# Performance work log

Measured on AMD Instinct MI355X. Metric: run time of the kernel, lower is better.

## Reference

```python
import jax, jax.numpy as jnp
import numpy as np

N_NODES = 100000
N_EDGES = 1600000
D_IN = 64
D_HID = 64


def setup_inputs() -> dict:
    key = jax.random.key(0)
    ks = jax.random.split(key, 9)
    feat = jax.random.uniform(ks[0], (N_NODES, D_IN), dtype=jnp.float32) + 1e-3
    edge_index = jax.random.randint(ks[1], (2, N_EDGES), 0, N_NODES, dtype=jnp.int64)
    edge_vals = jax.random.uniform(ks[2], (N_EDGES,), dtype=jnp.float32) + 1e-3
    W1 = jax.random.normal(ks[3], (D_IN, D_HID), dtype=jnp.float32) * 0.1
    b1 = jax.random.normal(ks[4], (D_HID,), dtype=jnp.float32) * 0.1
    W2 = jax.random.normal(ks[5], (D_HID, D_HID), dtype=jnp.float32) * 0.1
    b2 = jax.random.normal(ks[6], (D_HID,), dtype=jnp.float32) * 0.1
    W3 = jax.random.normal(ks[7], (D_HID, 1), dtype=jnp.float32) * 0.1
    b3 = jax.random.normal(ks[8], (1,), dtype=jnp.float32) * 0.1
    return {"feat": feat, "edge_index": edge_index, "edge_vals": edge_vals,
            "W1": W1, "b1": b1, "W2": W2, "b2": b2, "W3": W3, "b3": b3}


def reference(feat, edge_index, edge_vals, W1, b1, W2, b2, W3, b3):
    N = feat.shape[0]
    src = edge_index[0]
    dst = edge_index[1]
    # --- __init__: A_hat = D^{-1} A D^{-1}, D = diag(row sums of A) ---
    deg_row = jax.ops.segment_sum(edge_vals, src, num_segments=N)
    deg_row = jnp.where(deg_row > 0, deg_row, 1.0)  # guard isolated nodes
    w_hat = edge_vals / (deg_row[src] * deg_row[dst])  # A_hat edge weights
    # --- GCNConv gcn_norm: add self loops (weight 1), symmetric D^{-1/2} norm ---
    loops = jnp.arange(N, dtype=src.dtype)
    row = jnp.concatenate([src, loops])   # message sources
    col = jnp.concatenate([dst, loops])   # message targets (aggregation index)
    w = jnp.concatenate([w_hat, jnp.ones((N,), dtype=feat.dtype)])
    deg = jax.ops.segment_sum(w, col, num_segments=N)
    dinv = jnp.where(deg > 0, jax.lax.rsqrt(deg), 0.0)
    norm = dinv[row] * w * dinv[col]      # [E+N]

    def gcn_conv(x, W, b):
        h = x @ W                          # [N, d_out]
        msg = norm[:, None] * h[row]       # gather + scale, [E+N, d_out]
        return jax.ops.segment_sum(msg, col, num_segments=N) + b

    # --- forward ---
    x = feat / jnp.sum(feat, axis=1, keepdims=True)
    x = jax.nn.relu(gcn_conv(x, W1, b1))
    x = jax.nn.relu(gcn_conv(x, W2, b2))
    x = gcn_conv(x, W3, b3)               # final layer, no activation
    return x
```

## Files before the change

### kernel.cpp

```cpp
#include <hip/hip_runtime.h>
#include <hip/hip_fp16.h>


#define CAP    48
#define NRL    256
#define NBMX   512
#define P0E    2048

#define PG     2048

__device__ __forceinline__ float dec_ev(unsigned pk) {
    return __half2float(__ushort_as_half((unsigned short)(pk >> 17)));
}
__device__ __forceinline__ float dec_ev15(unsigned pk) {
    return __half2float(__ushort_as_half((unsigned short)(pk & 0x7FFF)));
}

__global__ __launch_bounds__(256) void k_scatter(
        const int* __restrict__ src, const int* __restrict__ dst,
        const float* __restrict__ ev,
        int* __restrict__ meta_d, int2* __restrict__ part_blk,
        int* __restrict__ meta_s, int* __restrict__ parts_src,
        int E, int NB) {
    __shared__ int2 srt[P0E];
    __shared__ int  srs[P0E];
    __shared__ int hd[NBMX], cbd[NBMX], lod[NBMX];
    __shared__ int hs[NBMX], cbs[NBMX], los[NBMX];
    int bx = (int)blockIdx.x, tid = (int)threadIdx.x;
    int e0 = bx * P0E;
    int ne = E - e0; if (ne > P0E) ne = P0E; if (ne < 0) ne = 0;
    for (int i = tid; i < NB; i += 256) { hd[i] = 0; hs[i] = 0; }
    __syncthreads();
    for (int i = tid; i < ne; i += 256) {
        atomicAdd(&hd[dst[e0 + i] >> 8], 1);
        atomicAdd(&hs[src[e0 + i] >> 8], 1);
    }
    __syncthreads();
    int wv = tid >> 6, ln = tid & 63;
    if (wv < 2) {
        int* h  = wv ? hs  : hd;
        int* cb = wv ? cbs : cbd;
        int run = 0;
        #pragma unroll
        for (int k = 0; k < NBMX / 64; k++) {
            int idx = k * 64 + ln;
            int v = (idx < NB) ? h[idx] : 0;
            int sc = v;
            #pragma unroll
            for (int o = 1; o < 64; o <<= 1) {
                int u = __shfl_up(sc, o, 64);
                if (ln >= o) sc += u;
            }
            if (idx < NB) cb[idx] = run + sc - v;
            run += __shfl(sc, 63, 64);
        }
    }
    __syncthreads();
    for (int c = tid; c < NB; c += 256) {
        lod[c] = cbd[c];
        los[c] = cbs[c];
        meta_d[(size_t)bx * NB + c] = (cbd[c] << 16) | hd[c];
        meta_s[(size_t)bx * NB + c] = (cbs[c] << 16) | hs[c];
    }
    __syncthreads();
    for (int i = tid; i < ne; i += 256) {
        int e = e0 + i;
        int s = src[e], d = dst[e];
        float v = ev[e];
        unsigned evh = (unsigned)__half_as_ushort(__float2half_rn(v)) & 0x7FFF;
        int p = atomicAdd(&lod[d >> 8], 1);
        int2 r;
        r.x = ((d & (NRL - 1)) << 17) | s;
        r.y = __float_as_int(v);
        srt[p] = r;
        int q = atomicAdd(&los[s >> 8], 1);
        srs[q] = (int)(((unsigned)(s & (NRL - 1)) << 15) | evh);
    }
    __syncthreads();
    for (int i = tid; i < ne; i += 256) {
        part_blk[(size_t)bx * P0E + i]  = srt[i];
        parts_src[(size_t)bx * P0E + i] = srs[i];
    }
}

__global__ __launch_bounds__(256) void k_degacc(
        const int* __restrict__ parts_src, const int* __restrict__ meta_s,
        float* __restrict__ deg_row, int N, int NB, int nsb) {
    __shared__ float dl[NRL];
    int b = (int)blockIdx.x, tid = (int)threadIdx.x;
    if (tid < NRL) dl[tid] = 0.f;
    __syncthreads();
    for (int bx = tid; bx < nsb; bx += 256) {
        int m = meta_s[(size_t)bx * NB + b];
        int base = m >> 16, len = m & 0xFFFF;
        const int* seg = parts_src + (size_t)bx * P0E + base;
        for (int j = 0; j < len; j++) {
            unsigned pk = (unsigned)seg[j];
            atomicAdd(&dl[pk >> 15], dec_ev15(pk));
        }
    }
    __syncthreads();
    int node = (b << 8) + tid;
    if (tid < NRL && node < N) deg_row[node] = dl[tid];
}

__global__ __launch_bounds__(256) void k_gemm1(
        const float* __restrict__ feat, const float* __restrict__ W1,
        __half* __restrict__ B, int N) {
    int lane = threadIdx.x & 63;
    float w[64];
    #pragma unroll
    for (int k = 0; k < 64; k++) w[k] = W1[k * 64 + lane];
    int wid = (int)blockIdx.x * 4 + (threadIdx.x >> 6);
    const int nw = PG * 4;
    for (int node = wid; node < N; node += nw) {
        float v = feat[(size_t)node * 64 + lane];
        float s = v;
        #pragma unroll
        for (int o = 1; o < 64; o <<= 1) s += __shfl_xor(s, o, 64);
        int myb = __float_as_int(v / s);
        float a0 = 0.f, a1 = 0.f, a2 = 0.f, a3 = 0.f;
        #pragma unroll
        for (int k = 0; k < 64; k += 4) {
            a0 = fmaf(__int_as_float(__builtin_amdgcn_readlane(myb, k + 0)), w[k + 0], a0);
            a1 = fmaf(__int_as_float(__builtin_amdgcn_readlane(myb, k + 1)), w[k + 1], a1);
            a2 = fmaf(__int_as_float(__builtin_amdgcn_readlane(myb, k + 2)), w[k + 2], a2);
            a3 = fmaf(__int_as_float(__builtin_amdgcn_readlane(myb, k + 3)), w[k + 3], a3);
        }
        B[(size_t)node * 64 + lane] = __float2half((a0 + a1) + (a2 + a3));
    }
}

__global__ __launch_bounds__(256) void k_bucket(
        const int2* __restrict__ part_blk, const int* __restrict__ meta_d,
        const float* __restrict__ deg_row,
        int* __restrict__ cnt, int* __restrict__ epair,
        float* __restrict__ di_t, float* __restrict__ r_t,
        int N, int NB, int nsb) {
    __shared__ int   lbuck[NRL * CAP];
    __shared__ int   lcnt[NRL];
    __shared__ float lt[NRL];
    int b = (int)blockIdx.x, tid = (int)threadIdx.x;
    if (tid < NRL) { lcnt[tid] = 0; lt[tid] = 0.f; }
    __syncthreads();
    for (int bx = tid; bx < nsb; bx += 256) {
        int m = meta_d[(size_t)bx * NB + b];
        int base = m >> 16, len = m & 0xFFFF;
        const int2* seg = part_blk + (size_t)bx * P0E + base;
        for (int j = 0; j < len; j++) {
            int2 r = seg[j];
            int dl = (r.x >> 17) & (NRL - 1);
            int s  = r.x & 0x1FFFF;
            float v = __int_as_float(r.y);
            atomicAdd(&lt[dl], v / deg_row[s]);
            unsigned evh = (unsigned)__half_as_ushort(__float2half_rn(v)) & 0x7FFF;
            int p = atomicAdd(&lcnt[dl], 1);
            if (p < CAP) lbuck[dl * CAP + p] = (int)((evh << 17) | (unsigned)s);
        }
    }
    __syncthreads();
    int node0 = b << 8;
    if (tid < NRL) {
        int node = node0 + tid;
        if (node < N) {
            int c = lcnt[tid]; if (c > CAP) c = CAP;
            cnt[node] = c;
            float drd = deg_row[node];
            drd = drd > 0.f ? drd : 1.f;
            float qd = 1.0f / drd;
            float di = rsqrtf(1.0f + qd * lt[tid]);
            di_t[node] = di;
            r_t[node]  = qd * di;
        }
    }
    __syncthreads();
    size_t base = (size_t)node0 * CAP;
    for (int i = tid; i < NRL * CAP; i += 256) epair[base + i] = lbuck[i];
}

__global__ __launch_bounds__(256) void k_p3(const int* __restrict__ cnt,
                                            int* __restrict__ epair,
                                            const float* __restrict__ r_t, int N) {
    int lane = threadIdx.x & 63;
    int node = blockIdx.x * 4 + (threadIdx.x >> 6);
    if (node >= N) return;
    int c = cnt[node]; if (c > CAP) c = CAP;
    if (lane < c) {
        size_t o = (size_t)node * CAP + lane;
        unsigned e = (unsigned)epair[o];
        int s = (int)(e & 0x1FFFF);
        float w = dec_ev(e) * r_t[s];
        unsigned wh = (unsigned)__half_as_ushort(__float2half_rn(w)) & 0x7FFF;
        epair[o] = (int)((wh << 17) | (unsigned)s);
    }
}

__device__ __forceinline__ void gather8(int c, int rec,
        const __half* __restrict__ h, int grp, int sub, float acc[8]) {
    #pragma unroll
    for (int q = 0; q < 8; q++) acc[q] = 0.f;
    int nb = (c + 7) >> 3;
    for (int t = 0; t < nb; t += 2) {
        int r0 = __shfl(rec, (t << 3) + grp, 64);
        int s0 = r0 & 0x1FFFF;
        float w0 = dec_ev((unsigned)r0);
        uint4 d0 = *reinterpret_cast<const uint4*>(h + ((size_t)s0 << 6) + (sub << 3));
        bool have1 = (t + 1 < nb);
        uint4 d1; float w1 = 0.f;
        if (have1) {
            int r1 = __shfl(rec, (t << 3) + 8 + grp, 64);
            int s1 = r1 & 0x1FFFF;
            w1 = dec_ev((unsigned)r1);
            d1 = *reinterpret_cast<const uint4*>(h + ((size_t)s1 << 6) + (sub << 3));
        }
        {
            const __half2* p0 = reinterpret_cast<const __half2*>(&d0);
            #pragma unroll
            for (int q = 0; q < 4; q++) {
                float2 f = __half22float2(p0[q]);
                acc[2 * q]     = fmaf(w0, f.x, acc[2 * q]);
                acc[2 * q + 1] = fmaf(w0, f.y, acc[2 * q + 1]);
            }
        }
        if (have1) {
            const __half2* p1 = reinterpret_cast<const __half2*>(&d1);
            #pragma unroll
            for (int q = 0; q < 4; q++) {
                float2 f = __half22float2(p1[q]);
                acc[2 * q]     = fmaf(w1, f.x, acc[2 * q]);
                acc[2 * q + 1] = fmaf(w1, f.y, acc[2 * q + 1]);
            }
        }
    }
    #pragma unroll
    for (int o = 8; o < 64; o <<= 1) {
        #pragma unroll
        for (int q = 0; q < 8; q++)
            acc[q] += __shfl_xor(acc[q], o, 64);
    }
}

__global__ __launch_bounds__(256) void k_gath1(
        const int* __restrict__ cnt, const int* __restrict__ epair,
        const __half* __restrict__ B,
        const float* __restrict__ di_t, const float* __restrict__ r_t,
        const float* __restrict__ b1, __half* __restrict__ X2, int N) {
    int lane = threadIdx.x & 63;
    int grp = lane >> 3, sub = lane & 7;
    int node = (int)blockIdx.x * 4 + (threadIdx.x >> 6);
    if (node >= N) return;
    int un = __builtin_amdgcn_readfirstlane(node);
    int c  = __builtin_amdgcn_readfirstlane(cnt[un]);
    if (c > CAP) c = CAP;
    int rec = 0;
    if (lane < c) rec = epair[(size_t)un * CAP + lane];
    uint4 dow = *reinterpret_cast<const uint4*>(B + ((size_t)un << 6) + (sub << 3));
    float g[8];
    gather8(c, rec, B, grp, sub, g);
    float di = di_t[un], rd = r_t[un];
    float dd = di * di;
    const float4* b4 = reinterpret_cast<const float4*>(b1);
    float4 bA = b4[sub * 2], bB = b4[sub * 2 + 1];
    const __half2* po = reinterpret_cast<const __half2*>(&dow);
    float2 o0 = __half22float2(po[0]), o1 = __half22float2(po[1]);
    float2 o2 = __half22float2(po[2]), o3 = __half22float2(po[3]);
    float x0 = fmaxf(bA.x + dd * o0.x + rd * g[0], 0.f);
    float x1 = fmaxf(bA.y + dd * o0.y + rd * g[1], 0.f);
    float x2 = fmaxf(bA.z + dd * o1.x + rd * g[2], 0.f);
    float x3 = fmaxf(bA.w + dd * o1.y + rd * g[3], 0.f);
    float x4 = fmaxf(bB.x + dd * o2.x + rd * g[4], 0.f);
    float x5 = fmaxf(bB.y + dd * o2.y + rd * g[5], 0.f);
    float x6 = fmaxf(bB.z + dd * o3.x + rd * g[6], 0.f);
    float x7 = fmaxf(bB.w + dd * o3.y + rd * g[7], 0.f);
    if (grp == 0) {
        __half2 h0 = __floats2half2_rn(x0, x1);
        __half2 h1 = __floats2half2_rn(x2, x3);
        __half2 h2 = __floats2half2_rn(x4, x5);
        __half2 h3 = __floats2half2_rn(x6, x7);
        uint4 ov;
        ov.x = *reinterpret_cast<unsigned*>(&h0);
        ov.y = *reinterpret_cast<unsigned*>(&h1);
        ov.z = *reinterpret_cast<unsigned*>(&h2);
        ov.w = *reinterpret_cast<unsigned*>(&h3);
        *reinterpret_cast<uint4*>(X2 + ((size_t)un << 6) + (sub << 3)) = ov;
    }
}

__global__ __launch_bounds__(256) void k_gemm2(
        const __half* __restrict__ X2, const float* __restrict__ W2,
        __half* __restrict__ C, int N) {
    int lane = threadIdx.x & 63;
    float w[64];
    #pragma unroll
    for (int k = 0; k < 64; k++) w[k] = W2[k * 64 + lane];
    int wid = (int)blockIdx.x * 4 + (threadIdx.x >> 6);
    const int nw = PG * 4;
    for (int node = wid; node < N; node += nw) {
        int myb = __float_as_int(__half2float(X2[(size_t)node * 64 + lane]));
        float a0 = 0.f, a1 = 0.f, a2 = 0.f, a3 = 0.f;
        #pragma unroll
        for (int k = 0; k < 64; k += 4) {
            a0 = fmaf(__int_as_float(__builtin_amdgcn_readlane(myb, k + 0)), w[k + 0], a0);
            a1 = fmaf(__int_as_float(__builtin_amdgcn_readlane(myb, k + 1)), w[k + 1], a1);
            a2 = fmaf(__int_as_float(__builtin_amdgcn_readlane(myb, k + 2)), w[k + 2], a2);
            a3 = fmaf(__int_as_float(__builtin_amdgcn_readlane(myb, k + 3)), w[k + 3], a3);
        }
        C[(size_t)node * 64 + lane] = __float2half((a0 + a1) + (a2 + a3));
    }
}

__global__ __launch_bounds__(256) void k_gather_dot(
        const int* __restrict__ cnt, const int* __restrict__ epair,
        const __half* __restrict__ C,
        const float* __restrict__ di_t, const float* __restrict__ r_t,
        const float* __restrict__ b2, const float* __restrict__ W3,
        float* __restrict__ h3, int N) {
    int lane = threadIdx.x & 63;
    int grp = lane >> 3, sub = lane & 7;
    int node = (int)blockIdx.x * 4 + (threadIdx.x >> 6);
    if (node >= N) return;
    int un = __builtin_amdgcn_readfirstlane(node);
    int c  = __builtin_amdgcn_readfirstlane(cnt[un]);
    if (c > CAP) c = CAP;
    int rec = 0;
    if (lane < c) rec = epair[(size_t)un * CAP + lane];
    uint4 dow = *reinterpret_cast<const uint4*>(C + ((size_t)un << 6) + (sub << 3));
    float g[8];
    gather8(c, rec, C, grp, sub, g);
    float di = di_t[un], rd = r_t[un];
    float dd = di * di;
    const float4* b4 = reinterpret_cast<const float4*>(b2);
    const float4* w4 = reinterpret_cast<const float4*>(W3);
    float4 bA = b4[sub * 2], bB = b4[sub * 2 + 1];
    float4 wA = w4[sub * 2], wB = w4[sub * 2 + 1];
    const __half2* po = reinterpret_cast<const __half2*>(&dow);
    float2 o0 = __half22float2(po[0]), o1 = __half22float2(po[1]);
    float2 o2 = __half22float2(po[2]), o3 = __half22float2(po[3]);
    float pd = 0.f;
    pd += fmaxf(bA.x + dd * o0.x + rd * g[0], 0.f) * wA.x;
    pd += fmaxf(bA.y + dd * o0.y + rd * g[1], 0.f) * wA.y;
    pd += fmaxf(bA.z + dd * o1.x + rd * g[2], 0.f) * wA.z;
    pd += fmaxf(bA.w + dd * o1.y + rd * g[3], 0.f) * wA.w;
    pd += fmaxf(bB.x + dd * o2.x + rd * g[4], 0.f) * wB.x;
    pd += fmaxf(bB.y + dd * o2.y + rd * g[5], 0.f) * wB.y;
    pd += fmaxf(bB.z + dd * o3.x + rd * g[6], 0.f) * wB.z;
    pd += fmaxf(bB.w + dd * o3.y + rd * g[7], 0.f) * wB.w;
    #pragma unroll
    for (int o = 1; o < 8; o <<= 1) pd += __shfl_xor(pd, o, 64);
    if (lane == 0) h3[un] = pd;
}

__global__ __launch_bounds__(256) void k_gather1(const int* __restrict__ cnt,
                                                 const int* __restrict__ epair,
                                                 const float* __restrict__ h3,
                                                 const float* __restrict__ di_t,
                                                 const float* __restrict__ r_t,
                                                 const float* __restrict__ b3,
                                                 float* __restrict__ out, int N) {
    int lane = threadIdx.x & 63;
    int node = blockIdx.x * 4 + (threadIdx.x >> 6);
    if (node >= N) return;
    int c = cnt[node]; if (c > CAP) c = CAP;
    float e0 = 0.f;
    if (lane < c) {
        unsigned pk = (unsigned)epair[(size_t)node * CAP + lane];
        e0 = dec_ev(pk) * h3[pk & 0x1FFFF];
    }
    #pragma unroll
    for (int o = 1; o < 64; o <<= 1) e0 += __shfl_xor(e0, o, 64);
    if (lane == 0) {
        float di = di_t[node];
        out[node] = b3[0] + di * di * h3[node] + r_t[node] * e0;
    }
}

extern "C" void kernel_launch(void* const* d_in, const int* in_sizes, int n_in,
                              void* d_out, int out_size, void* d_ws, size_t ws_size,
                              hipStream_t stream) {
    const float* feat = (const float*)d_in[0];
    const int*   eidx = (const int*)d_in[1];
    const float* ev   = (const float*)d_in[2];
    const float* W1 = (const float*)d_in[3];
    const float* b1 = (const float*)d_in[4];
    const float* W2 = (const float*)d_in[5];
    const float* b2 = (const float*)d_in[6];
    const float* W3 = (const float*)d_in[7];
    const float* b3 = (const float*)d_in[8];

    const int N = in_sizes[0] / 64;
    const int E = in_sizes[2];
    const int* src = eidx;
    const int* dst = eidx + E;
    const int NB   = (N + NRL - 1) / NRL;
    const int npad = NB * NRL;
    const int nsb  = (E + P0E - 1) / P0E;

    char* p = (char*)d_ws;
    auto carve = [&](size_t nbytes) { char* r = p; p += (nbytes + 255) & ~(size_t)255; return r; };
    float*    deg_row   = (float*)   carve((size_t)N * 4);
    float*    di_t      = (float*)   carve((size_t)N * 4);
    float*    r_t       = (float*)   carve((size_t)N * 4);
    float*    h3        = (float*)   carve((size_t)N * 4);
    int*      cnt       = (int*)     carve((size_t)npad * 4);
    int*      meta_d    = (int*)     carve((size_t)nsb * NB * 4);
    int*      meta_s    = (int*)     carve((size_t)nsb * NB * 4);
    int*      epair     = (int*)     carve((size_t)npad * CAP * 4);
    int2*     part_blk  = (int2*)    carve((size_t)nsb * P0E * 8);
    int*      parts_src = (int*)     carve((size_t)nsb * P0E * 4);
    __half*   B         = (__half*)  carve((size_t)N * 64 * 2);
    __half*   X2        = (__half*)part_blk;
    __half*   C         = (__half*)B;
    float*    out       = (float*)d_out;

    const int BLK = 256;
    int gNode4 = (N + 3) / 4;

    k_scatter   <<<nsb, BLK, 0, stream>>>(src, dst, ev, meta_d, part_blk,
                                          meta_s, parts_src, E, NB);
    k_degacc    <<<NB, BLK, 0, stream>>>(parts_src, meta_s, deg_row, N, NB, nsb);
    k_gemm1     <<<PG, BLK, 0, stream>>>(feat, W1, B, N);
    k_bucket    <<<NB, BLK, 0, stream>>>(part_blk, meta_d, deg_row, cnt, epair,
                                         di_t, r_t, N, NB, nsb);
    k_p3        <<<gNode4, BLK, 0, stream>>>(cnt, epair, r_t, N);

    k_gath1     <<<gNode4, BLK, 0, stream>>>(cnt, epair, B, di_t, r_t, b1, X2, N);
    k_gemm2     <<<PG, BLK, 0, stream>>>(X2, W2, C, N);
    k_gather_dot<<<gNode4, BLK, 0, stream>>>(cnt, epair, C, di_t, r_t,
                                             b2, W3, h3, N);
    k_gather1   <<<gNode4, BLK, 0, stream>>>(cnt, epair, h3, di_t, r_t, b3, out, N);
}
```

Measured before the change: 327.9 us.

## Process eight nodes per wavefront in layer-1/2 gathers with 8 lanes per node

The two 64-wide gather kernels now map eight nodes to each wavefront, with eight lanes per node each holding 8 features. Previously a whole wavefront handled one node and reduced partial sums across lane groups. Each lane group now walks its node's neighbor list in blocks of eight, issuing eight independent 16-byte loads per block. Loop trip count is set by the largest degree in the wavefront. This drops the cross-group shuffle reduction, wastes fewer lanes on low-degree nodes and exposes more memory-level parallelism, at the cost of idle lanes when degrees are unbalanced and more registers.

```diff
diff --git a/kernel.cpp b/kernel.cpp
--- a/kernel.cpp
+++ b/kernel.cpp
@@ -195,88 +195,100 @@
     }
 }
 
-__device__ __forceinline__ void gather8(int c, int rec,
-        const __half* __restrict__ h, int grp, int sub, float acc[8]) {
+__device__ __forceinline__ void gt_fma8(const uint4& d, float w, float acc[8]) {
+    const __half2* p = reinterpret_cast<const __half2*>(&d);
     #pragma unroll
-    for (int q = 0; q < 8; q++) acc[q] = 0.f;
-    int nb = (c + 7) >> 3;
-    for (int t = 0; t < nb; t += 2) {
-        int r0 = __shfl(rec, (t << 3) + grp, 64);
-        int s0 = r0 & 0x1FFFF;
-        float w0 = dec_ev((unsigned)r0);
-        uint4 d0 = *reinterpret_cast<const uint4*>(h + ((size_t)s0 << 6) + (sub << 3));
-        bool have1 = (t + 1 < nb);
-        uint4 d1; float w1 = 0.f;
-        if (have1) {
-            int r1 = __shfl(rec, (t << 3) + 8 + grp, 64);
-            int s1 = r1 & 0x1FFFF;
-            w1 = dec_ev((unsigned)r1);
-            d1 = *reinterpret_cast<const uint4*>(h + ((size_t)s1 << 6) + (sub << 3));
-        }
-        {
-            const __half2* p0 = reinterpret_cast<const __half2*>(&d0);
-            #pragma unroll
-            for (int q = 0; q < 4; q++) {
-                float2 f = __half22float2(p0[q]);
-                acc[2 * q]     = fmaf(w0, f.x, acc[2 * q]);
-                acc[2 * q + 1] = fmaf(w0, f.y, acc[2 * q + 1]);
-            }
-        }
-        if (have1) {
-            const __half2* p1 = reinterpret_cast<const __half2*>(&d1);
-            #pragma unroll
-            for (int q = 0; q < 4; q++) {
-                float2 f = __half22float2(p1[q]);
-                acc[2 * q]     = fmaf(w1, f.x, acc[2 * q]);
-                acc[2 * q + 1] = fmaf(w1, f.y, acc[2 * q + 1]);
-            }
-        }
-    }
-    #pragma unroll
-    for (int o = 8; o < 64; o <<= 1) {
-        #pragma unroll
-        for (int q = 0; q < 8; q++)
-            acc[q] += __shfl_xor(acc[q], o, 64);
-    }
-}
+    for (int q = 0; q < 4; q++) {
+        float2 f = __half22float2(p[q]);
+        acc[2 * q]     = fmaf(w, f.x, acc[2 * q]);
+        acc[2 * q + 1] = fmaf(w, f.y, acc[2 * q + 1]);
+    }
+}
+
+__device__ __forceinline__ void gt_block(int recr, int gb,
+        const __half* __restrict__ hp, float acc[8]) {
+    int e0 = __shfl(recr, gb + 0, 64);
+    int e1 = __shfl(recr, gb + 1, 64);
+    int e2 = __shfl(recr, gb + 2, 64);
+    int e3 = __shfl(recr, gb + 3, 64);
+    int e4 = __shfl(recr, gb + 4, 64);
+    int e5 = __shfl(recr, gb + 5, 64);
+    int e6 = __shfl(recr, gb + 6, 64);
+    int e7 = __shfl(recr, gb + 7, 64);
+    uint4 d0 = *reinterpret_cast<const uint4*>(hp + ((size_t)(e0 & 0x1FFFF) << 6));
+    uint4 d1 = *reinterpret_cast<const uint4*>(hp + ((size_t)(e1 & 0x1FFFF) << 6));
+    uint4 d2 = *reinterpret_cast<const uint4*>(hp + ((size_t)(e2 & 0x1FFFF) << 6));
+    uint4 d3 = *reinterpret_cast<const uint4*>(hp + ((size_t)(e3 & 0x1FFFF) << 6));
+    uint4 d4 = *reinterpret_cast<const uint4*>(hp + ((size_t)(e4 & 0x1FFFF) << 6));
+    uint4 d5 = *reinterpret_cast<const uint4*>(hp + ((size_t)(e5 & 0x1FFFF) << 6));
+    uint4 d6 = *reinterpret_cast<const uint4*>(hp + ((size_t)(e6 & 0x1FFFF) << 6));
+    uint4 d7 = *reinterpret_cast<const uint4*>(hp + ((size_t)(e7 & 0x1FFFF) << 6));
+    gt_fma8(d0, dec_ev((unsigned)e0), acc);
+    gt_fma8(d1, dec_ev((unsigned)e1), acc);
+    gt_fma8(d2, dec_ev((unsigned)e2), acc);
+    gt_fma8(d3, dec_ev((unsigned)e3), acc);
+    gt_fma8(d4, dec_ev((unsigned)e4), acc);
+    gt_fma8(d5, dec_ev((unsigned)e5), acc);
+    gt_fma8(d6, dec_ev((unsigned)e6), acc);
+    gt_fma8(d7, dec_ev((unsigned)e7), acc);
+}
+
+#define GT_PROLOGUE(cntp, epairp)                                            \
+    int lane = (int)threadIdx.x & 63;                                        \
+    int grp = lane >> 3, sub = lane & 7;                                     \
+    int base = (((int)blockIdx.x << 2) + ((int)threadIdx.x >> 6)) << 3;      \
+    int un = base + grp;                                                     \
+    int unc = un < N ? un : N - 1;                                           \
+    int c = un < N ? cntp[unc] : 0;                                          \
+    if (c > CAP) c = CAP;                                                    \
+    const int* ep = epairp + (size_t)unc * CAP + sub;                        \
+    int rec0 = 0, rec1 = 0, rec2 = 0, rec3 = 0, rec4 = 0, rec5 = 0;          \
+    if (sub + 0  < c) rec0 = ep[0];                                          \
+    if (sub + 8  < c) rec1 = ep[8];                                          \
+    if (sub + 16 < c) rec2 = ep[16];                                         \
+    if (sub + 24 < c) rec3 = ep[24];                                         \
+    if (sub + 32 < c) rec4 = ep[32];                                         \
+    if (sub + 40 < c) rec5 = ep[40];                                         \
+    int m = c;                                                               \
+    { int u;                                                                 \
+      u = __shfl_xor(m, 8, 64);  m = m > u ? m : u;                          \
+      u = __shfl_xor(m, 16, 64); m = m > u ? m : u;                          \
+      u = __shfl_xor(m, 32, 64); m = m > u ? m : u; }                        \
+    float acc[8];                                                            \
+    _Pragma("unroll")                                                        \
+    for (int q = 0; q < 8; q++) acc[q] = 0.f;                                \
+    int gb = grp << 3;
 
 __global__ __launch_bounds__(256) void k_gath1(
         const int* __restrict__ cnt, const int* __restrict__ epair,
         const __half* __restrict__ B,
         const float* __restrict__ di_t, const float* __restrict__ r_t,
         const float* __restrict__ b1, __half* __restrict__ X2, int N) {
-    int lane = threadIdx.x & 63;
-    int grp = lane >> 3, sub = lane & 7;
-    int node = (int)blockIdx.x * 4 + (threadIdx.x >> 6);
-    if (node >= N) return;
-    int un = __builtin_amdgcn_readfirstlane(node);
-    int c  = __builtin_amdgcn_readfirstlane(cnt[un]);
-    if (c > CAP) c = CAP;
-    int rec = 0;
-    if (lane < c) rec = epair[(size_t)un * CAP + lane];
-    uint4 dow = *reinterpret_cast<const uint4*>(B + ((size_t)un << 6) + (sub << 3));
-    float g[8];
-    gather8(c, rec, B, grp, sub, g);
-    float di = di_t[un], rd = r_t[un];
+    GT_PROLOGUE(cnt, epair)
+    const __half* hp = B + (sub << 3);
+    uint4 dow = *reinterpret_cast<const uint4*>(B + ((size_t)unc << 6) + (sub << 3));
+    gt_block(rec0, gb, hp, acc);
+    if (m > 8)  gt_block(rec1, gb, hp, acc);
+    if (m > 16) gt_block(rec2, gb, hp, acc);
+    if (m > 24) gt_block(rec3, gb, hp, acc);
+    if (m > 32) gt_block(rec4, gb, hp, acc);
+    if (m > 40) gt_block(rec5, gb, hp, acc);
+    float di = di_t[unc], rd = r_t[unc];
     float dd = di * di;
     const float4* b4 = reinterpret_cast<const float4*>(b1);
     float4 bA = b4[sub * 2], bB = b4[sub * 2 + 1];
     const __half2* po = reinterpret_cast<const __half2*>(&dow);
     float2 o0 = __half22float2(po[0]), o1 = __half22float2(po[1]);
     float2 o2 = __half22float2(po[2]), o3 = __half22float2(po[3]);
-    float x0 = fmaxf(bA.x + dd * o0.x + rd * g[0], 0.f);
-    float x1 = fmaxf(bA.y + dd * o0.y + rd * g[1], 0.f);
-    float x2 = fmaxf(bA.z + dd * o1.x + rd * g[2], 0.f);
-    float x3 = fmaxf(bA.w + dd * o1.y + rd * g[3], 0.f);
-    float x4 = fmaxf(bB.x + dd * o2.x + rd * g[4], 0.f);
-    float x5 = fmaxf(bB.y + dd * o2.y + rd * g[5], 0.f);
-    float x6 = fmaxf(bB.z + dd * o3.x + rd * g[6], 0.f);
-    float x7 = fmaxf(bB.w + dd * o3.y + rd * g[7], 0.f);
-    if (grp == 0) {
-        __half2 h0 = __floats2half2_rn(x0, x1);
-        __half2 h1 = __floats2half2_rn(x2, x3);
-        __half2 h2 = __floats2half2_rn(x4, x5);
-        __half2 h3 = __floats2half2_rn(x6, x7);
+    __half2 h0 = __floats2half2_rn(fmaxf(bA.x + dd * o0.x + rd * acc[0], 0.f),
+                                   fmaxf(bA.y + dd * o0.y + rd * acc[1], 0.f));
+    __half2 h1 = __floats2half2_rn(fmaxf(bA.z + dd * o1.x + rd * acc[2], 0.f),
+                                   fmaxf(bA.w + dd * o1.y + rd * acc[3], 0.f));
+    __half2 h2 = __floats2half2_rn(fmaxf(bB.x + dd * o2.x + rd * acc[4], 0.f),
+                                   fmaxf(bB.y + dd * o2.y + rd * acc[5], 0.f));
+    __half2 h3 = __floats2half2_rn(fmaxf(bB.z + dd * o3.x + rd * acc[6], 0.f),
+                                   fmaxf(bB.w + dd * o3.y + rd * acc[7], 0.f));
+    if (un < N) {
         uint4 ov;
         ov.x = *reinterpret_cast<unsigned*>(&h0);
         ov.y = *reinterpret_cast<unsigned*>(&h1);
@@ -315,19 +327,16 @@
         const float* __restrict__ di_t, const float* __restrict__ r_t,
         const float* __restrict__ b2, const float* __restrict__ W3,
         float* __restrict__ h3, int N) {
-    int lane = threadIdx.x & 63;
-    int grp = lane >> 3, sub = lane & 7;
-    int node = (int)blockIdx.x * 4 + (threadIdx.x >> 6);
-    if (node >= N) return;
-    int un = __builtin_amdgcn_readfirstlane(node);
-    int c  = __builtin_amdgcn_readfirstlane(cnt[un]);
-    if (c > CAP) c = CAP;
-    int rec = 0;
-    if (lane < c) rec = epair[(size_t)un * CAP + lane];
-    uint4 dow = *reinterpret_cast<const uint4*>(C + ((size_t)un << 6) + (sub << 3));
-    float g[8];
-    gather8(c, rec, C, grp, sub, g);
-    float di = di_t[un], rd = r_t[un];
+    GT_PROLOGUE(cnt, epair)
+    const __half* hp = C + (sub << 3);
+    uint4 dow = *reinterpret_cast<const uint4*>(C + ((size_t)unc << 6) + (sub << 3));
+    gt_block(rec0, gb, hp, acc);
+    if (m > 8)  gt_block(rec1, gb, hp, acc);
+    if (m > 16) gt_block(rec2, gb, hp, acc);
+    if (m > 24) gt_block(rec3, gb, hp, acc);
+    if (m > 32) gt_block(rec4, gb, hp, acc);
+    if (m > 40) gt_block(rec5, gb, hp, acc);
+    float di = di_t[unc], rd = r_t[unc];
     float dd = di * di;
     const float4* b4 = reinterpret_cast<const float4*>(b2);
     const float4* w4 = reinterpret_cast<const float4*>(W3);
@@ -337,17 +346,18 @@
     float2 o0 = __half22float2(po[0]), o1 = __half22float2(po[1]);
     float2 o2 = __half22float2(po[2]), o3 = __half22float2(po[3]);
     float pd = 0.f;
-    pd += fmaxf(bA.x + dd * o0.x + rd * g[0], 0.f) * wA.x;
-    pd += fmaxf(bA.y + dd * o0.y + rd * g[1], 0.f) * wA.y;
-    pd += fmaxf(bA.z + dd * o1.x + rd * g[2], 0.f) * wA.z;
-    pd += fmaxf(bA.w + dd * o1.y + rd * g[3], 0.f) * wA.w;
-    pd += fmaxf(bB.x + dd * o2.x + rd * g[4], 0.f) * wB.x;
-    pd += fmaxf(bB.y + dd * o2.y + rd * g[5], 0.f) * wB.y;
-    pd += fmaxf(bB.z + dd * o3.x + rd * g[6], 0.f) * wB.z;
-    pd += fmaxf(bB.w + dd * o3.y + rd * g[7], 0.f) * wB.w;
-    #pragma unroll
-    for (int o = 1; o < 8; o <<= 1) pd += __shfl_xor(pd, o, 64);
-    if (lane == 0) h3[un] = pd;
+    pd += fmaxf(bA.x + dd * o0.x + rd * acc[0], 0.f) * wA.x;
+    pd += fmaxf(bA.y + dd * o0.y + rd * acc[1], 0.f) * wA.y;
+    pd += fmaxf(bA.z + dd * o1.x + rd * acc[2], 0.f) * wA.z;
+    pd += fmaxf(bA.w + dd * o1.y + rd * acc[3], 0.f) * wA.w;
+    pd += fmaxf(bB.x + dd * o2.x + rd * acc[4], 0.f) * wB.x;
+    pd += fmaxf(bB.y + dd * o2.y + rd * acc[5], 0.f) * wB.y;
+    pd += fmaxf(bB.z + dd * o3.x + rd * acc[6], 0.f) * wB.z;
+    pd += fmaxf(bB.w + dd * o3.y + rd * acc[7], 0.f) * wB.w;
+    pd += __shfl_xor(pd, 1, 64);
+    pd += __shfl_xor(pd, 2, 64);
+    pd += __shfl_xor(pd, 4, 64);
+    if (sub == 0 && un < N) h3[un] = pd;
 }
 
 __global__ __launch_bounds__(256) void k_gather1(const int* __restrict__ cnt,
@@ -413,7 +423,8 @@
     float*    out       = (float*)d_out;
 
     const int BLK = 256;
-    int gNode4 = (N + 3) / 4;
+    int gNode4  = (N + 3) / 4;
+    int gNode32 = (N + 31) / 32;
 
     k_scatter   <<<nsb, BLK, 0, stream>>>(src, dst, ev, meta_d, part_blk,
                                           meta_s, parts_src, E, NB);
@@ -423,9 +434,9 @@
                                          di_t, r_t, N, NB, nsb);
     k_p3        <<<gNode4, BLK, 0, stream>>>(cnt, epair, r_t, N);
 
-    k_gath1     <<<gNode4, BLK, 0, stream>>>(cnt, epair, B, di_t, r_t, b1, X2, N);
+    k_gath1     <<<gNode32, BLK, 0, stream>>>(cnt, epair, B, di_t, r_t, b1, X2, N);
     k_gemm2     <<<PG, BLK, 0, stream>>>(X2, W2, C, N);
-    k_gather_dot<<<gNode4, BLK, 0, stream>>>(cnt, epair, C, di_t, r_t,
-                                             b2, W3, h3, N);
+    k_gather_dot<<<gNode32, BLK, 0, stream>>>(cnt, epair, C, di_t, r_t,
+                                              b2, W3, h3, N);
     k_gather1   <<<gNode4, BLK, 0, stream>>>(cnt, epair, h3, di_t, r_t, b3, out, N);
 }
```

Result: faster. 305.0 us (-7.0%).
